# Performance work log

Hardware: AMD Instinct MI355X
Metric: run time of the kernel (lower is better)

The kernel has to match this reference:

```python
import jax, jax.numpy as jnp
import numpy as np

MP_LAYERS = 3
PROPBETA = 0.05


def setup_inputs() -> dict:
    key = jax.random.key(0)
    k1, k2, k3, k4, k5, k6 = jax.random.split(key, 6)
    B, N, S, D = 32, 64, 336, 32
    x = jax.random.normal(k1, (B, N, S), dtype=jnp.float32)
    adj = jax.random.uniform(k2, (B, S, N, N), dtype=jnp.float32)
    # row-normalize like Graph_constructor output (rows sum to 1)
    adj = adj / jnp.sum(adj, axis=-1, keepdims=True)
    w_start = jax.random.normal(k3, (1, D), dtype=jnp.float32) / jnp.sqrt(1.0)
    b_start = jax.random.normal(k4, (D,), dtype=jnp.float32) * 0.01
    w_mlp = jax.random.normal(k5, ((MP_LAYERS + 1) * D, 1), dtype=jnp.float32) / jnp.sqrt((MP_LAYERS + 1) * D)
    b_mlp = jax.random.normal(k6, (1,), dtype=jnp.float32) * 0.01
    return {"x": x, "adj": adj, "w_start": w_start, "b_start": b_start,
            "w_mlp": w_mlp, "b_mlp": b_mlp}


def reference(x, adj, w_start, b_start, w_mlp, b_mlp):
    # x: [b, n, s]; adj: [b, s, n, m]
    a = jnp.transpose(adj, (0, 2, 3, 1))           # [b, n, m, s]
    xu = x[..., None]                               # [b, n, s, 1]
    h = jnp.einsum('bnsc,cd->bnsd', xu, w_start) + b_start  # startmlp
    out = [h]
    for _ in range(MP_LAYERS):
        conv = jnp.einsum('bnsc,bnms->bmsc', h, a)  # nconv
        h = PROPBETA * xu + (1.0 - PROPBETA) * conv
        out.append(h)
    h = jnp.concatenate(out, axis=-1)               # [b, n, s, (K+1)*d]
    h = jnp.einsum('bnsc,co->bnso', h, w_mlp) + b_mlp
    return h[..., 0]                                # [b, n, s]
```

## Files before the change

### kernel.cpp

```cpp
#include <hip/hip_runtime.h>


#define BB 32
#define NN 64
#define SS 336
#define DD 32
#define BETA 0.05f
#define OMB 0.95f

__global__ __launch_bounds__(256) void dgra_collapsed_kernel(
    const float* __restrict__ x, const float* __restrict__ adj,
    const float* __restrict__ w_start, const float* __restrict__ b_start,
    const float* __restrict__ w_mlp, const float* __restrict__ b_mlp,
    float* __restrict__ out)
{
    const int tid  = threadIdx.x;
    const int lane = tid & 63;
    const int w    = tid >> 6;
    const int blk  = blockIdx.x;
    const int b    = blk / (SS / 4);
    const int s4   = blk % (SS / 4);
    const int s    = s4 * 4 + w;

    float P[4] = {0.f,0.f,0.f,0.f}, Q[4] = {0.f,0.f,0.f,0.f}, R[4] = {0.f,0.f,0.f,0.f};
#pragma unroll
    for (int d = 0; d < DD; ++d) {
        const float wd = w_start[d];
        const float bd = b_start[d];
#pragma unroll
        for (int k = 0; k < 4; ++k) {
            const float m = w_mlp[k * DD + d];
            P[k] = fmaf(wd, m, P[k]);
            Q[k] = fmaf(bd, m, Q[k]);
            R[k] += m;
        }
    }
    float Pp[4];
    Pp[0] = P[0] + BETA * (R[1] + R[2] + R[3]);
    Pp[1] = P[1] + BETA * (R[2] + R[3]);
    Pp[2] = P[2] + BETA * R[3];
    Pp[3] = P[3];
    const float c0 = Q[0] + b_mlp[0];

    const float* Ab = adj + (size_t)(b * SS + s) * (NN * NN);
    float Areg[NN];
#pragma unroll
    for (int n = 0; n < NN; ++n)
        Areg[n] = Ab[n * NN + lane];

    float y = x[(size_t)(b * NN + lane) * SS + s];
    float u = 1.0f;
    float acc = fmaf(Pp[0], y, c0);

    __shared__ float2 yu[4][NN];

#pragma unroll
    for (int k = 1; k <= 3; ++k) {
        yu[w][lane] = make_float2(y, u);
        __asm__ volatile("s_waitcnt lgkmcnt(0)" ::: "memory");
        float ys = 0.f, us = 0.f;
#pragma unroll
        for (int n = 0; n < NN; ++n) {
            const float2 t = yu[w][n];
            ys = fmaf(Areg[n], t.x, ys);
            us = fmaf(Areg[n], t.y, us);
        }
        y = OMB * ys;
        u = OMB * us;
        acc = fmaf(Pp[k], y, acc);
        acc = fmaf(Q[k], u, acc);
    }

    __shared__ __align__(16) float res[NN][4];
    res[lane][w] = acc;
    __syncthreads();
    if (w == 0) {
        const float4 v = *reinterpret_cast<const float4*>(res[lane]);
        *reinterpret_cast<float4*>(&out[(size_t)(b * NN + lane) * SS + s4 * 4]) = v;
    }
}

extern "C" void kernel_launch(void* const* d_in, const int* in_sizes, int n_in,
                              void* d_out, int out_size, void* d_ws, size_t ws_size,
                              hipStream_t stream) {
    const float* x       = (const float*)d_in[0];
    const float* adj     = (const float*)d_in[1];
    const float* w_start = (const float*)d_in[2];
    const float* b_start = (const float*)d_in[3];
    const float* w_mlp   = (const float*)d_in[4];
    const float* b_mlp   = (const float*)d_in[5];
    float* out = (float*)d_out;

    const int grid = BB * (SS / 4);
    dgra_collapsed_kernel<<<grid, 256, 0, stream>>>(x, adj, w_start, b_start, w_mlp, b_mlp, out);
}
```

Measured before the change: 37.48 us.

## Stream adjacency through double-buffered LDS with direct global-to-LDS loads

Replaces the per-wave register-resident adjacency (64 floats per lane) with a 512-thread block that double-buffers four consecutive adj slices in LDS using global_load_lds_dwordx4, overlapping the next slice's load with the current propagation. The 64-term contraction is split across 8 waves, with partial sums reduced through shared memory, which adds several __syncthreads per hop. The weight pre-reduction is parallelised with cross-lane shuffles. The aim is lower register pressure, higher occupancy and overlapped memory traffic, at the cost of many more block barriers and a serialized walk over the four s values.

Measured after the change: 91.00 us. 143% more time.

```diff
diff --git a/kernel.cpp b/kernel.cpp
--- a/kernel.cpp
+++ b/kernel.cpp
@@ -8,7 +8,18 @@
 #define BETA 0.05f
 #define OMB 0.95f
 
-__global__ __launch_bounds__(256) void dgra_collapsed_kernel(
+#define VMWAIT2() asm volatile("s_waitcnt vmcnt(2)" ::: "memory")
+#define VMWAIT0() asm volatile("s_waitcnt vmcnt(0)" ::: "memory")
+
+__device__ __forceinline__ void glds_1kb(const float* gsrc, unsigned lds_byte_off) {
+    unsigned m0v = __builtin_amdgcn_readfirstlane(lds_byte_off);
+    asm volatile("s_mov_b32 m0, %0\n\t"
+                 "global_load_lds_dwordx4 %1, off\n\t"
+                 "s_mov_b32 m0, -1"
+                 :: "s"(m0v), "v"(gsrc) : "memory");
+}
+
+__global__ __launch_bounds__(512, 8) void dgra_pipe_kernel(
     const float* __restrict__ x, const float* __restrict__ adj,
     const float* __restrict__ w_start, const float* __restrict__ b_start,
     const float* __restrict__ w_mlp, const float* __restrict__ b_mlp,
@@ -17,66 +28,108 @@
     const int tid  = threadIdx.x;
     const int lane = tid & 63;
     const int w    = tid >> 6;
-    const int blk  = blockIdx.x;
-    const int b    = blk / (SS / 4);
-    const int s4   = blk % (SS / 4);
-    const int s    = s4 * 4 + w;
+    const int b    = blockIdx.x / (SS / 4);
+    const int s4   = blockIdx.x % (SS / 4);
+    const int s0   = s4 * 4;
 
-    float P[4] = {0.f,0.f,0.f,0.f}, Q[4] = {0.f,0.f,0.f,0.f}, R[4] = {0.f,0.f,0.f,0.f};
+    __shared__ __align__(16) float  Abuf[2][NN * NN];
+    __shared__ __align__(16) float2 part[8][NN];
+    __shared__ __align__(16) float2 yu[NN];
+
+    const float* Abase = adj + (size_t)(b * SS + s0) * (NN * NN);
+
+    const float4 xq = *reinterpret_cast<const float4*>(&x[(size_t)(b * NN + lane) * SS + s0]);
+    const float xj[4] = {xq.x, xq.y, xq.z, xq.w};
+
+    const unsigned buf0 = (unsigned)(uintptr_t)(&Abuf[0][0]) + (unsigned)(w * 2048);
+    const unsigned buf1 = (unsigned)(uintptr_t)(&Abuf[1][0]) + (unsigned)(w * 2048);
+
+    {
+        const float* g = Abase + w * 512 + lane * 4;
+        glds_1kb(g,       buf0);
+        glds_1kb(g + 256, buf0 + 1024);
+    }
+
+    const int  c2 = lane & 31;
+    const int  hi = lane >> 5;
+    const float wd  = w_start[c2];
+    const float bd  = b_start[c2];
+    const float m0f = w_mlp[(2 * hi + 0) * DD + c2];
+    const float m1f = w_mlp[(2 * hi + 1) * DD + c2];
+    float p0 = wd * m0f, q0 = bd * m0f, r0 = m0f;
+    float p1 = wd * m1f, q1 = bd * m1f, r1 = m1f;
 #pragma unroll
-    for (int d = 0; d < DD; ++d) {
-        const float wd = w_start[d];
-        const float bd = b_start[d];
+    for (int mask = 1; mask <= 16; mask <<= 1) {
+        p0 += __shfl_xor(p0, mask, 64);  q0 += __shfl_xor(q0, mask, 64);  r0 += __shfl_xor(r0, mask, 64);
+        p1 += __shfl_xor(p1, mask, 64);  q1 += __shfl_xor(q1, mask, 64);  r1 += __shfl_xor(r1, mask, 64);
+    }
+    const float po0 = __shfl_xor(p0, 32, 64), qo0 = __shfl_xor(q0, 32, 64), ro0 = __shfl_xor(r0, 32, 64);
+    const float po1 = __shfl_xor(p1, 32, 64), qo1 = __shfl_xor(q1, 32, 64), ro1 = __shfl_xor(r1, 32, 64);
+    const bool lo = (hi == 0);
+    const float P0 = lo ? p0  : po0, P1 = lo ? p1  : po1, P2 = lo ? po0 : p0, P3 = lo ? po1 : p1;
+    const float Q0 = lo ? q0  : qo0, Q1 = lo ? q1  : qo1, Q2 = lo ? qo0 : q0, Q3 = lo ? qo1 : q1;
+    const float R1 = lo ? r1  : ro1, R2 = lo ? ro0 : r0,  R3 = lo ? ro1 : r1;
+    const float PpA[4] = {P0 + BETA * (R1 + R2 + R3), P1 + BETA * (R2 + R3), P2 + BETA * R3, P3};
+    const float QA[4]  = {Q0, Q1, Q2, Q3};
+    const float c0f = Q0 + b_mlp[0];
+
+    if (w == 0) yu[lane] = make_float2(xj[0], 1.0f);
+    __syncthreads();
+
+    asm volatile("" :: "v"(xq.x), "v"(xq.y), "v"(xq.z), "v"(xq.w));
+
+    float acc[4];
+
 #pragma unroll
-        for (int k = 0; k < 4; ++k) {
-            const float m = w_mlp[k * DD + d];
-            P[k] = fmaf(wd, m, P[k]);
-            Q[k] = fmaf(bd, m, Q[k]);
-            R[k] += m;
+    for (int j = 0; j < 4; ++j) {
+        if (j < 3) {
+            const float* g = Abase + (j + 1) * 4096 + w * 512 + lane * 4;
+            const unsigned dst = ((j + 1) & 1) ? buf1 : buf0;
+            glds_1kb(g,       dst);
+            glds_1kb(g + 256, dst + 1024);
+            VMWAIT2();
+        } else {
+            VMWAIT0();
+        }
+
+        const float* Ab = &Abuf[j & 1][0];
+        float av[8];
+#pragma unroll
+        for (int i = 0; i < 8; ++i)
+            av[i] = Ab[(8 * w + i) * NN + lane];
+
+        acc[j] = fmaf(PpA[0], xj[j], c0f);
+
+#pragma unroll
+        for (int k = 1; k <= 3; ++k) {
+            float py = 0.f, pu = 0.f;
+#pragma unroll
+            for (int i = 0; i < 8; ++i) {
+                const float2 t = yu[8 * w + i];
+                py = fmaf(av[i], t.x, py);
+                pu = fmaf(av[i], t.y, pu);
+            }
+            part[w][lane] = make_float2(py, pu);
+            __syncthreads();
+            float ys = 0.f, us = 0.f;
+#pragma unroll
+            for (int p = 0; p < 8; ++p) {
+                const float2 t = part[p][lane];
+                ys += t.x; us += t.y;
+            }
+            ys *= OMB; us *= OMB;
+            acc[j] = fmaf(PpA[k], ys, fmaf(QA[k], us, acc[j]));
+            if (w == 0) {
+                if (k < 3)      yu[lane] = make_float2(ys, us);
+                else if (j < 3) yu[lane] = make_float2(xj[j + 1], 1.0f);
+            }
+            __syncthreads();
         }
     }
-    float Pp[4];
-    Pp[0] = P[0] + BETA * (R[1] + R[2] + R[3]);
-    Pp[1] = P[1] + BETA * (R[2] + R[3]);
-    Pp[2] = P[2] + BETA * R[3];
-    Pp[3] = P[3];
-    const float c0 = Q[0] + b_mlp[0];
 
-    const float* Ab = adj + (size_t)(b * SS + s) * (NN * NN);
-    float Areg[NN];
-#pragma unroll
-    for (int n = 0; n < NN; ++n)
-        Areg[n] = Ab[n * NN + lane];
-
-    float y = x[(size_t)(b * NN + lane) * SS + s];
-    float u = 1.0f;
-    float acc = fmaf(Pp[0], y, c0);
-
-    __shared__ float2 yu[4][NN];
-
-#pragma unroll
-    for (int k = 1; k <= 3; ++k) {
-        yu[w][lane] = make_float2(y, u);
-        __asm__ volatile("s_waitcnt lgkmcnt(0)" ::: "memory");
-        float ys = 0.f, us = 0.f;
-#pragma unroll
-        for (int n = 0; n < NN; ++n) {
-            const float2 t = yu[w][n];
-            ys = fmaf(Areg[n], t.x, ys);
-            us = fmaf(Areg[n], t.y, us);
-        }
-        y = OMB * ys;
-        u = OMB * us;
-        acc = fmaf(Pp[k], y, acc);
-        acc = fmaf(Q[k], u, acc);
-    }
-
-    __shared__ __align__(16) float res[NN][4];
-    res[lane][w] = acc;
-    __syncthreads();
     if (w == 0) {
-        const float4 v = *reinterpret_cast<const float4*>(res[lane]);
-        *reinterpret_cast<float4*>(&out[(size_t)(b * NN + lane) * SS + s4 * 4]) = v;
+        float4 o; o.x = acc[0]; o.y = acc[1]; o.z = acc[2]; o.w = acc[3];
+        *reinterpret_cast<float4*>(&out[(size_t)(b * NN + lane) * SS + s0]) = o;
     }
 }
 
@@ -92,5 +145,5 @@
     float* out = (float*)d_out;
 
     const int grid = BB * (SS / 4);
-    dgra_collapsed_kernel<<<grid, 256, 0, stream>>>(x, adj, w_start, b_start, w_mlp, b_mlp, out);
+    dgra_pipe_kernel<<<grid, 512, 0, stream>>>(x, adj, w_start, b_start, w_mlp, b_mlp, out);
 }
```
